# Kernel tuning notes

Hardware: AMD Instinct MI355X
Metric: run time of the kernel (lower is better)

## Reference

```python
import jax, jax.numpy as jnp
import numpy as np

N_NODES = 50000
N_EDGES = 800000
IN_CH = 128
HID_CH = 128   # 2 * out_channels
OUT_CH = 64


def setup_inputs() -> dict:
    key = jax.random.key(0)
    k1, k2, k3, k4 = jax.random.split(key, 4)
    x = jax.random.normal(k1, (N_NODES, IN_CH), dtype=jnp.float32)
    edge_index = jax.random.randint(k2, (2, N_EDGES), 0, N_NODES, dtype=jnp.int64)
    # Glorot-ish scaled weights
    W1 = jax.random.normal(k3, (IN_CH, HID_CH), dtype=jnp.float32) * (1.0 / np.sqrt(IN_CH))
    b1 = jnp.zeros((HID_CH,), dtype=jnp.float32)
    W2 = jax.random.normal(k4, (HID_CH, OUT_CH), dtype=jnp.float32) * (1.0 / np.sqrt(HID_CH))
    b2 = jnp.zeros((OUT_CH,), dtype=jnp.float32)
    return {"x": x, "edge_index": edge_index, "W1": W1, "b1": b1, "W2": W2, "b2": b2}


def _gcn_conv(x, src, dst, W, b):
    # PyG GCNConv: add self-loops, symmetric deg^-1/2 normalization,
    # linear transform, scatter-add aggregation, bias.
    n = x.shape[0]
    loop = jnp.arange(n, dtype=src.dtype)
    s = jnp.concatenate([src, loop])
    d = jnp.concatenate([dst, loop])
    ones = jnp.ones(s.shape[0], dtype=x.dtype)
    deg = jax.ops.segment_sum(ones, d, num_segments=n)  # [N]
    dinv = jnp.where(deg > 0, deg ** -0.5, 0.0)
    norm = dinv[s] * dinv[d]                             # [E+N]
    xw = x @ W                                           # [N, F_out]
    msg = xw[s] * norm[:, None]                          # gather + scale
    agg = jax.ops.segment_sum(msg, d, num_segments=n)    # scatter-add
    return agg + b


def reference(x, edge_index, W1, b1, W2, b2):
    src, dst = edge_index[0], edge_index[1]
    h = jax.nn.relu(_gcn_conv(x, src, dst, W1, b1))
    out = jax.nn.relu(_gcn_conv(h, src, dst, W2, b2))
    return out
```

## Files before the change

### kernel.cpp

```cpp
#include <hip/hip_runtime.h>
#include <hip/hip_fp16.h>

using half8 = __attribute__((ext_vector_type(8))) _Float16;
using f32x4 = __attribute__((ext_vector_type(4))) float;

#define MAXB 256
#define ECAP 5376
#define EPB  3200
#define XHB  192


__global__ void prep(const float* __restrict__ W1, const float* __restrict__ W2,
                     _Float16* __restrict__ W1p, _Float16* __restrict__ W2p,
                     int* __restrict__ bktcnt) {
    int tid = threadIdx.x;
    if (blockIdx.x == 0) bktcnt[tid] = 0;
    int idx = blockIdx.x * 256 + tid;
    if (idx < 32 * 512) {
        int f = idx >> 9, rem = idx & 511, l = rem >> 3, j = rem & 7;
        int kt = f >> 3, nt = f & 7;
        W1p[idx] = (_Float16)W1[(kt * 32 + (l >> 4) * 8 + j) * 128 + nt * 16 + (l & 15)];
    } else if (idx < 32 * 512 + 16 * 512) {
        int i2 = idx - 32 * 512;
        int f = i2 >> 9, rem = i2 & 511, l = rem >> 3, j = rem & 7;
        int kt = f >> 2, nt = f & 3;
        W2p[i2] = (_Float16)W2[(kt * 32 + (l >> 4) * 8 + j) * 64 + nt * 16 + (l & 15)];
    }
}


__global__ __launch_bounds__(256) void bin_xh(const int* __restrict__ src,
                                              const int* __restrict__ dst,
                                              int* __restrict__ bktcnt,
                                              unsigned int* __restrict__ entries,
                                              const float* __restrict__ x,
                                              __half2* __restrict__ xh,
                                              int E, int N, int binBlocks) {
    int tid = threadIdx.x;
    if ((int)blockIdx.x >= binBlocks) {
        int n32 = N * 32;
        for (int idx = ((int)blockIdx.x - binBlocks) * 256 + tid; idx < n32; idx += XHB * 256) {
            float4 xv = *(const float4*)&x[(size_t)idx * 4];
            uint2 o;
            __half2 h0 = __float22half2_rn(make_float2(xv.x, xv.y));
            __half2 h1 = __float22half2_rn(make_float2(xv.z, xv.w));
            __builtin_memcpy(&o.x, &h0, 4);
            __builtin_memcpy(&o.y, &h1, 4);
            *(uint2*)&xh[(size_t)idx * 2] = o;
        }
        return;
    }

    __shared__ unsigned int ebuf[EPB];
    __shared__ unsigned char bbuf[EPB];
    __shared__ int cntL[MAXB], fillL[MAXB], baseL[MAXB];
    cntL[tid] = 0;
    __syncthreads();

    int e0 = blockIdx.x * EPB;
    int e1 = min(e0 + EPB, E);
    int m = e1 - e0;

    for (int i = tid; i < m; i += 256) {
        int e = e0 + i;
        int s = src[e], d = dst[e];
        int b = 0;
        unsigned int entry = 0xFFFFFFFFu;
        if ((unsigned)s < (unsigned)N && (unsigned)d < (unsigned)N) {
            b = d >> 8;
            entry = (unsigned)s | ((unsigned)(d & 255) << 16);
            atomicAdd(&cntL[b], 1);
        }
        ebuf[i] = entry;
        bbuf[i] = (unsigned char)b;
    }
    __syncthreads();

    int c = cntL[tid];
    if (c > 0) baseL[tid] = atomicAdd(&bktcnt[tid], c);
    fillL[tid] = 0;
    __syncthreads();

    for (int i = tid; i < m; i += 256) {
        unsigned int entry = ebuf[i];
        if (entry == 0xFFFFFFFFu) continue;
        int b = bbuf[i];
        int pos = atomicAdd(&fillL[b], 1);
        int idx = baseL[b] + pos;
        if (idx < ECAP) entries[(size_t)b * ECAP + idx] = entry;
    }
}


__global__ __launch_bounds__(256) void build_csr(const unsigned int* __restrict__ entries,
                                                 const int* __restrict__ bktcnt,
                                                 int* __restrict__ rowp, int* __restrict__ cnt,
                                                 float* __restrict__ dinv,
                                                 unsigned short* __restrict__ col_src,
                                                 int N, int nbkt) {
    __shared__ int sb[256];
    __shared__ int cntL[256], offL[256], fillL[256];
    int b = blockIdx.x, tid = threadIdx.x;

    int bv = (tid < nbkt) ? min(bktcnt[tid], ECAP) : 0;
    sb[tid] = bv;
    cntL[tid] = 0;
    __syncthreads();
    for (int off = 1; off < 256; off <<= 1) {
        int t = (tid >= off) ? sb[tid - off] : 0;
        __syncthreads();
        sb[tid] += t;
        __syncthreads();
    }
    int tot = min(bktcnt[b], ECAP);
    int base = sb[b] - tot;

    const unsigned int* sp = entries + (size_t)b * ECAP;
    for (int i = tid; i < tot; i += 256) atomicAdd(&cntL[(sp[i] >> 16) & 255], 1);
    __syncthreads();

    int v = cntL[tid];
    offL[tid] = v;
    __syncthreads();
    for (int off = 1; off < 256; off <<= 1) {
        int t = (tid >= off) ? offL[tid - off] : 0;
        __syncthreads();
        offL[tid] += t;
        __syncthreads();
    }

    int ex = offL[tid] - v;
    int node = (b << 8) + tid;
    if (node < N) {
        rowp[node] = base + ex;
        cnt[node]  = v;
        dinv[node] = rsqrtf((float)(v + 1));
    }
    fillL[tid] = ex;
    __syncthreads();

    for (int i = tid; i < tot; i += 256) {
        unsigned int e = sp[i];
        int slot = atomicAdd(&fillL[(e >> 16) & 255], 1);
        col_src[base + slot] = (unsigned short)(e & 0xFFFFu);
    }
}


__global__ void agg_x128_h(const __half2* __restrict__ x2, const int* __restrict__ rowp,
                           const int* __restrict__ cnt, const unsigned short* __restrict__ col,
                           const float* __restrict__ dinv, __half2* __restrict__ out2, int n) {
    int node = blockIdx.x * 4 + (threadIdx.x >> 6);
    if (node >= n) return;
    int lane = threadIdx.x & 63;
    float di = dinv[node];
    float2 self = __half22float2(x2[(size_t)node * 64 + lane]);
    float ax[8], ay[8];
    ax[0] = di * self.x; ay[0] = di * self.y;
#pragma unroll
    for (int j = 1; j < 8; ++j) { ax[j] = 0.f; ay[j] = 0.f; }
    int p = rowp[node];
    int deg = cnt[node];
    int k = 0;
    for (; k + 16 <= deg; k += 16) {
        int s[16];
#pragma unroll
        for (int j = 0; j < 16; ++j) s[j] = col[p + k + j];
        float ds[16];
#pragma unroll
        for (int j = 0; j < 16; ++j) ds[j] = dinv[s[j]];
        float2 v[16];
#pragma unroll
        for (int j = 0; j < 16; ++j) v[j] = __half22float2(x2[(size_t)s[j] * 64 + lane]);
#pragma unroll
        for (int j = 0; j < 16; ++j) { ax[j & 7] += ds[j] * v[j].x; ay[j & 7] += ds[j] * v[j].y; }
    }
    if (k + 8 <= deg) {
        int s[8];
#pragma unroll
        for (int j = 0; j < 8; ++j) s[j] = col[p + k + j];
        float ds[8];
#pragma unroll
        for (int j = 0; j < 8; ++j) ds[j] = dinv[s[j]];
        float2 v[8];
#pragma unroll
        for (int j = 0; j < 8; ++j) v[j] = __half22float2(x2[(size_t)s[j] * 64 + lane]);
#pragma unroll
        for (int j = 0; j < 8; ++j) { ax[j] += ds[j] * v[j].x; ay[j] += ds[j] * v[j].y; }
        k += 8;
    }
    if (k + 4 <= deg) {
        int s[4];
#pragma unroll
        for (int j = 0; j < 4; ++j) s[j] = col[p + k + j];
        float ds[4];
#pragma unroll
        for (int j = 0; j < 4; ++j) ds[j] = dinv[s[j]];
        float2 v[4];
#pragma unroll
        for (int j = 0; j < 4; ++j) v[j] = __half22float2(x2[(size_t)s[j] * 64 + lane]);
#pragma unroll
        for (int j = 0; j < 4; ++j) { ax[j] += ds[j] * v[j].x; ay[j] += ds[j] * v[j].y; }
        k += 4;
    }
    for (; k < deg; ++k) {
        int s = col[p + k];
        float dsv = dinv[s];
        float2 v = __half22float2(x2[(size_t)s * 64 + lane]);
        ax[0] += dsv * v.x; ay[0] += dsv * v.y;
    }
    float axs = ((ax[0] + ax[1]) + (ax[2] + ax[3])) + ((ax[4] + ax[5]) + (ax[6] + ax[7]));
    float ays = ((ay[0] + ay[1]) + (ay[2] + ay[3])) + ((ay[4] + ay[5]) + (ay[6] + ay[7]));
    __half2 o = __float22half2_rn(make_float2(di * axs, di * ays));
    unsigned int ob;
    __builtin_memcpy(&ob, &o, 4);
    __builtin_nontemporal_store(ob, (unsigned int*)&out2[(size_t)node * 64 + lane]);
}


__global__ __launch_bounds__(256) void mlp_mfma(const _Float16* __restrict__ axh,
                                                const _Float16* __restrict__ W1p,
                                                const float* __restrict__ b1,
                                                const _Float16* __restrict__ W2p,
                                                const float* __restrict__ dinv,
                                                _Float16* __restrict__ yh, int M) {
    __shared__ _Float16 sh[4][16][136];
    int t = threadIdx.x;
    int w = t >> 6, l = t & 63;
    int rlo = l & 15, khi = l >> 4;
    int row0 = blockIdx.x * 64 + w * 16;

    half8 a[4];
    int arow = row0 + rlo;
    const half8* arp = (const half8*)(axh + (size_t)arow * 128 + khi * 8);
#pragma unroll
    for (int kt = 0; kt < 4; ++kt) {
        half8 v = {};
        if (arow < M) v = __builtin_nontemporal_load(arp + kt * 4);
        a[kt] = v;
    }

    f32x4 acc[8];
#pragma unroll
    for (int nt = 0; nt < 8; ++nt) acc[nt] = (f32x4){0.f, 0.f, 0.f, 0.f};
#pragma unroll
    for (int nt = 0; nt < 8; ++nt) {
#pragma unroll
        for (int kt = 0; kt < 4; ++kt) {
            half8 b = *(const half8*)&W1p[(size_t)((kt * 8 + nt) * 64 + l) * 8];
            acc[nt] = __builtin_amdgcn_mfma_f32_16x16x32_f16(a[kt], b, acc[nt], 0, 0, 0);
        }
    }

#pragma unroll
    for (int nt = 0; nt < 8; ++nt) {
        float bb = b1[nt * 16 + rlo];
#pragma unroll
        for (int r = 0; r < 4; ++r)
            sh[w][khi * 4 + r][nt * 16 + rlo] = (_Float16)fmaxf(acc[nt][r] + bb, 0.f);
    }
    __syncthreads();

    half8 a2[4];
#pragma unroll
    for (int kt = 0; kt < 4; ++kt)
        a2[kt] = *(const half8*)&sh[w][rlo][kt * 32 + khi * 8];

    f32x4 acc2[4];
#pragma unroll
    for (int nt = 0; nt < 4; ++nt) acc2[nt] = (f32x4){0.f, 0.f, 0.f, 0.f};
#pragma unroll
    for (int nt = 0; nt < 4; ++nt) {
#pragma unroll
        for (int kt = 0; kt < 4; ++kt) {
            half8 b = *(const half8*)&W2p[(size_t)((kt * 4 + nt) * 64 + l) * 8];
            acc2[nt] = __builtin_amdgcn_mfma_f32_16x16x32_f16(a2[kt], b, acc2[nt], 0, 0, 0);
        }
    }

#pragma unroll
    for (int r = 0; r < 4; ++r) {
        int row = row0 + khi * 4 + r;
        if (row < M) {
            float dn = dinv[row];
#pragma unroll
            for (int nt = 0; nt < 4; ++nt)
                yh[(size_t)row * 64 + nt * 16 + rlo] = (_Float16)(acc2[nt][r] * dn);
        }
    }
}


__global__ void agg_y64_h(const __half* __restrict__ y, const int* __restrict__ rowp,
                          const int* __restrict__ cnt, const unsigned short* __restrict__ col,
                          const float* __restrict__ dinv, const float* __restrict__ bias,
                          float* __restrict__ out, int n) {
    int node = blockIdx.x * 4 + (threadIdx.x >> 6);
    if (node >= n) return;
    int lane = threadIdx.x & 63;
    const __half* yc = y + lane;
    float a[8];
    a[0] = __half2float(yc[(size_t)node * 64]);
#pragma unroll
    for (int j = 1; j < 8; ++j) a[j] = 0.f;
    int p = rowp[node];
    int deg = cnt[node];
    int k = 0;
    for (; k + 16 <= deg; k += 16) {
        float v[16];
#pragma unroll
        for (int j = 0; j < 16; ++j) v[j] = __half2float(yc[(size_t)col[p + k + j] * 64]);
#pragma unroll
        for (int j = 0; j < 16; ++j) a[j & 7] += v[j];
    }
    if (k + 8 <= deg) {
        float v[8];
#pragma unroll
        for (int j = 0; j < 8; ++j) v[j] = __half2float(yc[(size_t)col[p + k + j] * 64]);
#pragma unroll
        for (int j = 0; j < 8; ++j) a[j] += v[j];
        k += 8;
    }
    if (k + 4 <= deg) {
        float v[4];
#pragma unroll
        for (int j = 0; j < 4; ++j) v[j] = __half2float(yc[(size_t)col[p + k + j] * 64]);
#pragma unroll
        for (int j = 0; j < 4; ++j) a[j] += v[j];
        k += 4;
    }
    for (; k < deg; ++k) a[0] += __half2float(yc[(size_t)col[p + k] * 64]);
    float as = ((a[0] + a[1]) + (a[2] + a[3])) + ((a[4] + a[5]) + (a[6] + a[7]));
    float o = fmaxf(bias[lane] + dinv[node] * as, 0.f);
    __builtin_nontemporal_store(o, &out[(size_t)node * 64 + lane]);
}


extern "C" void kernel_launch(void* const* d_in, const int* in_sizes, int n_in,
                              void* d_out, int out_size, void* d_ws, size_t ws_size,
                              hipStream_t stream) {
    const float* x  = (const float*)d_in[0];
    const int*   ei = (const int*)d_in[1];
    const float* W1 = (const float*)d_in[2];
    const float* b1 = (const float*)d_in[3];
    const float* W2 = (const float*)d_in[4];
    const float* b2 = (const float*)d_in[5];
    float* out = (float*)d_out;

    const int N = in_sizes[0] / 128;
    const int E = in_sizes[1] / 2;
    const int nbkt = (N + 255) >> 8;
    const int* src = ei;
    const int* dst = ei + E;

    char* ws = (char*)d_ws;
    size_t off = 0;
    auto alloc = [&](size_t bytes) {
        void* p = ws + off;
        off += (bytes + 255) & ~(size_t)255;
        return p;
    };
    int*            bktcnt  = (int*)           alloc((size_t)MAXB * 4);
    int*            rowp    = (int*)           alloc((size_t)N * 4);
    int*            cnt     = (int*)           alloc((size_t)N * 4);
    float*          dinv    = (float*)         alloc((size_t)N * 4);
    unsigned int*   entries = (unsigned int*)  alloc((size_t)nbkt * ECAP * 4);
    unsigned short* col_src = (unsigned short*)alloc((size_t)E * 2);
    __half2*        xh      = (__half2*)       alloc((size_t)N * 128 * 2);
    __half2*        axh     = (__half2*)       alloc((size_t)N * 128 * 2);
    __half2*        yh      = (__half2*)       alloc((size_t)N * 64 * 2);
    _Float16*       W1p     = (_Float16*)      alloc((size_t)32 * 512 * 2);
    _Float16*       W2p     = (_Float16*)      alloc((size_t)16 * 512 * 2);

    const int binBlocks = (E + EPB - 1) / EPB;

    prep<<<96, 256, 0, stream>>>(W1, W2, W1p, W2p, bktcnt);
    bin_xh<<<binBlocks + XHB, 256, 0, stream>>>(src, dst, bktcnt, entries, x, xh, E, N, binBlocks);
    build_csr<<<nbkt, 256, 0, stream>>>(entries, bktcnt, rowp, cnt, dinv, col_src, N, nbkt);
    agg_x128_h<<<(N + 3) / 4, 256, 0, stream>>>(xh, rowp, cnt, col_src, dinv, axh, N);
    mlp_mfma<<<(N + 63) / 64, 256, 0, stream>>>((const _Float16*)axh, W1p, b1, W2p, dinv,
                                                (_Float16*)yh, N);
    agg_y64_h<<<(N + 3) / 4, 256, 0, stream>>>((const __half*)yh, rowp, cnt, col_src, dinv, b2, out, N);
}
```

Baseline: 115.7 us.

## Fuse layer-1 aggregation into MFMA MLP kernel via per-wave LDS tile

Merges the first-layer neighbor aggregation into the MLP kernel. Each wave now aggregates 16 nodes one after another and writes the half-precision results into a per-wave LDS tile, which then feeds the MFMA A operands directly. This removes the global axh intermediate (its write and read back) and one kernel launch. The block barrier goes away because all LDS data is private to each wave. In exchange the gather runs on far fewer waves, each looping serially over 16 nodes, and the block uses more LDS, so latency hiding for the irregular gathers may drop.

```diff
diff --git a/kernel.cpp b/kernel.cpp
--- a/kernel.cpp
+++ b/kernel.cpp
@@ -147,98 +147,95 @@
 }
 
 
-__global__ void agg_x128_h(const __half2* __restrict__ x2, const int* __restrict__ rowp,
-                           const int* __restrict__ cnt, const unsigned short* __restrict__ col,
-                           const float* __restrict__ dinv, __half2* __restrict__ out2, int n) {
-    int node = blockIdx.x * 4 + (threadIdx.x >> 6);
-    if (node >= n) return;
-    int lane = threadIdx.x & 63;
-    float di = dinv[node];
-    float2 self = __half22float2(x2[(size_t)node * 64 + lane]);
-    float ax[8], ay[8];
-    ax[0] = di * self.x; ay[0] = di * self.y;
-#pragma unroll
-    for (int j = 1; j < 8; ++j) { ax[j] = 0.f; ay[j] = 0.f; }
-    int p = rowp[node];
-    int deg = cnt[node];
-    int k = 0;
-    for (; k + 16 <= deg; k += 16) {
-        int s[16];
-#pragma unroll
-        for (int j = 0; j < 16; ++j) s[j] = col[p + k + j];
-        float ds[16];
-#pragma unroll
-        for (int j = 0; j < 16; ++j) ds[j] = dinv[s[j]];
-        float2 v[16];
-#pragma unroll
-        for (int j = 0; j < 16; ++j) v[j] = __half22float2(x2[(size_t)s[j] * 64 + lane]);
-#pragma unroll
-        for (int j = 0; j < 16; ++j) { ax[j & 7] += ds[j] * v[j].x; ay[j & 7] += ds[j] * v[j].y; }
-    }
-    if (k + 8 <= deg) {
-        int s[8];
-#pragma unroll
-        for (int j = 0; j < 8; ++j) s[j] = col[p + k + j];
-        float ds[8];
-#pragma unroll
-        for (int j = 0; j < 8; ++j) ds[j] = dinv[s[j]];
-        float2 v[8];
-#pragma unroll
-        for (int j = 0; j < 8; ++j) v[j] = __half22float2(x2[(size_t)s[j] * 64 + lane]);
-#pragma unroll
-        for (int j = 0; j < 8; ++j) { ax[j] += ds[j] * v[j].x; ay[j] += ds[j] * v[j].y; }
-        k += 8;
-    }
-    if (k + 4 <= deg) {
-        int s[4];
-#pragma unroll
-        for (int j = 0; j < 4; ++j) s[j] = col[p + k + j];
-        float ds[4];
-#pragma unroll
-        for (int j = 0; j < 4; ++j) ds[j] = dinv[s[j]];
-        float2 v[4];
-#pragma unroll
-        for (int j = 0; j < 4; ++j) v[j] = __half22float2(x2[(size_t)s[j] * 64 + lane]);
-#pragma unroll
-        for (int j = 0; j < 4; ++j) { ax[j] += ds[j] * v[j].x; ay[j] += ds[j] * v[j].y; }
-        k += 4;
-    }
-    for (; k < deg; ++k) {
-        int s = col[p + k];
-        float dsv = dinv[s];
-        float2 v = __half22float2(x2[(size_t)s * 64 + lane]);
-        ax[0] += dsv * v.x; ay[0] += dsv * v.y;
-    }
-    float axs = ((ax[0] + ax[1]) + (ax[2] + ax[3])) + ((ax[4] + ax[5]) + (ax[6] + ax[7]));
-    float ays = ((ay[0] + ay[1]) + (ay[2] + ay[3])) + ((ay[4] + ay[5]) + (ay[6] + ay[7]));
-    __half2 o = __float22half2_rn(make_float2(di * axs, di * ays));
-    unsigned int ob;
-    __builtin_memcpy(&ob, &o, 4);
-    __builtin_nontemporal_store(ob, (unsigned int*)&out2[(size_t)node * 64 + lane]);
-}
-
-
-__global__ __launch_bounds__(256) void mlp_mfma(const _Float16* __restrict__ axh,
+__global__ __launch_bounds__(256) void agg1_mlp(const __half2* __restrict__ x2,
+                                                const int* __restrict__ rowp,
+                                                const int* __restrict__ cnt,
+                                                const unsigned short* __restrict__ col,
+                                                const float* __restrict__ dinv,
+                                                const float* __restrict__ b1,
                                                 const _Float16* __restrict__ W1p,
-                                                const float* __restrict__ b1,
                                                 const _Float16* __restrict__ W2p,
-                                                const float* __restrict__ dinv,
-                                                _Float16* __restrict__ yh, int M) {
+                                                _Float16* __restrict__ yh, int n) {
+    __shared__ _Float16 axL[4][16][136];
     __shared__ _Float16 sh[4][16][136];
     int t = threadIdx.x;
     int w = t >> 6, l = t & 63;
+    int node0 = blockIdx.x * 64 + w * 16;
+
+    for (int r = 0; r < 16; ++r) {
+        int node = node0 + r;
+        __half2 o;
+        if (node < n) {
+            float di = dinv[node];
+            float2 self = __half22float2(x2[(size_t)node * 64 + l]);
+            float ax[8], ay[8];
+            ax[0] = di * self.x; ay[0] = di * self.y;
+#pragma unroll
+            for (int j = 1; j < 8; ++j) { ax[j] = 0.f; ay[j] = 0.f; }
+            int p = rowp[node];
+            int deg = cnt[node];
+            int k = 0;
+            for (; k + 16 <= deg; k += 16) {
+                int s[16];
+#pragma unroll
+                for (int j = 0; j < 16; ++j) s[j] = col[p + k + j];
+                float ds[16];
+#pragma unroll
+                for (int j = 0; j < 16; ++j) ds[j] = dinv[s[j]];
+                float2 v[16];
+#pragma unroll
+                for (int j = 0; j < 16; ++j) v[j] = __half22float2(x2[(size_t)s[j] * 64 + l]);
+#pragma unroll
+                for (int j = 0; j < 16; ++j) { ax[j & 7] += ds[j] * v[j].x; ay[j & 7] += ds[j] * v[j].y; }
+            }
+            if (k + 8 <= deg) {
+                int s[8];
+#pragma unroll
+                for (int j = 0; j < 8; ++j) s[j] = col[p + k + j];
+                float ds[8];
+#pragma unroll
+                for (int j = 0; j < 8; ++j) ds[j] = dinv[s[j]];
+                float2 v[8];
+#pragma unroll
+                for (int j = 0; j < 8; ++j) v[j] = __half22float2(x2[(size_t)s[j] * 64 + l]);
+#pragma unroll
+                for (int j = 0; j < 8; ++j) { ax[j] += ds[j] * v[j].x; ay[j] += ds[j] * v[j].y; }
+                k += 8;
+            }
+            if (k + 4 <= deg) {
+                int s[4];
+#pragma unroll
+                for (int j = 0; j < 4; ++j) s[j] = col[p + k + j];
+                float ds[4];
+#pragma unroll
+                for (int j = 0; j < 4; ++j) ds[j] = dinv[s[j]];
+                float2 v[4];
+#pragma unroll
+                for (int j = 0; j < 4; ++j) v[j] = __half22float2(x2[(size_t)s[j] * 64 + l]);
+#pragma unroll
+                for (int j = 0; j < 4; ++j) { ax[j] += ds[j] * v[j].x; ay[j] += ds[j] * v[j].y; }
+                k += 4;
+            }
+            for (; k < deg; ++k) {
+                int s = col[p + k];
+                float dsv = dinv[s];
+                float2 v = __half22float2(x2[(size_t)s * 64 + l]);
+                ax[0] += dsv * v.x; ay[0] += dsv * v.y;
+            }
+            float axs = ((ax[0] + ax[1]) + (ax[2] + ax[3])) + ((ax[4] + ax[5]) + (ax[6] + ax[7]));
+            float ays = ((ay[0] + ay[1]) + (ay[2] + ay[3])) + ((ay[4] + ay[5]) + (ay[6] + ay[7]));
+            o = __float22half2_rn(make_float2(di * axs, di * ays));
+        } else {
+            o = __float22half2_rn(make_float2(0.f, 0.f));
+        }
+        *(__half2*)&axL[w][r][l * 2] = o;
+    }
+
     int rlo = l & 15, khi = l >> 4;
-    int row0 = blockIdx.x * 64 + w * 16;
-
     half8 a[4];
-    int arow = row0 + rlo;
-    const half8* arp = (const half8*)(axh + (size_t)arow * 128 + khi * 8);
-#pragma unroll
-    for (int kt = 0; kt < 4; ++kt) {
-        half8 v = {};
-        if (arow < M) v = __builtin_nontemporal_load(arp + kt * 4);
-        a[kt] = v;
-    }
+#pragma unroll
+    for (int kt = 0; kt < 4; ++kt)
+        a[kt] = *(const half8*)&axL[w][rlo][kt * 32 + khi * 8];
 
     f32x4 acc[8];
 #pragma unroll
@@ -259,7 +256,6 @@
         for (int r = 0; r < 4; ++r)
             sh[w][khi * 4 + r][nt * 16 + rlo] = (_Float16)fmaxf(acc[nt][r] + bb, 0.f);
     }
-    __syncthreads();
 
     half8 a2[4];
 #pragma unroll
@@ -280,8 +276,8 @@
 
 #pragma unroll
     for (int r = 0; r < 4; ++r) {
-        int row = row0 + khi * 4 + r;
-        if (row < M) {
+        int row = node0 + khi * 4 + r;
+        if (row < n) {
             float dn = dinv[row];
 #pragma unroll
             for (int nt = 0; nt < 4; ++nt)
@@ -367,7 +363,6 @@
     unsigned int*   entries = (unsigned int*)  alloc((size_t)nbkt * ECAP * 4);
     unsigned short* col_src = (unsigned short*)alloc((size_t)E * 2);
     __half2*        xh      = (__half2*)       alloc((size_t)N * 128 * 2);
-    __half2*        axh     = (__half2*)       alloc((size_t)N * 128 * 2);
     __half2*        yh      = (__half2*)       alloc((size_t)N * 64 * 2);
     _Float16*       W1p     = (_Float16*)      alloc((size_t)32 * 512 * 2);
     _Float16*       W2p     = (_Float16*)      alloc((size_t)16 * 512 * 2);
@@ -377,8 +372,7 @@
     prep<<<96, 256, 0, stream>>>(W1, W2, W1p, W2p, bktcnt);
     bin_xh<<<binBlocks + XHB, 256, 0, stream>>>(src, dst, bktcnt, entries, x, xh, E, N, binBlocks);
     build_csr<<<nbkt, 256, 0, stream>>>(entries, bktcnt, rowp, cnt, dinv, col_src, N, nbkt);
-    agg_x128_h<<<(N + 3) / 4, 256, 0, stream>>>(xh, rowp, cnt, col_src, dinv, axh, N);
-    mlp_mfma<<<(N + 63) / 64, 256, 0, stream>>>((const _Float16*)axh, W1p, b1, W2p, dinv,
+    agg1_mlp<<<(N + 63) / 64, 256, 0, stream>>>(xh, rowp, cnt, col_src, dinv, b1, W1p, W2p,
                                                 (_Float16*)yh, N);
     agg_y64_h<<<(N + 3) / 4, 256, 0, stream>>>((const __half*)yh, rowp, cnt, col_src, dinv, b2, out, N);
 }
```

Result: slower. 125.0 us (+8.0%).
